# Performance work log

Hardware: AMD Instinct MI355X
Metric: run time of the kernel (lower is better)

## Reference

```python
import jax, jax.numpy as jnp
import numpy as np

D_MODEL = 2048
N_HEADS = 16
N_KV_HEADS = 4
HEAD_DIM = D_MODEL // N_HEADS  # 128
ROPE_THETA = 1000000.0


def _quant_rowwise(x):
    """Symmetric int8 rowwise quantization over the last dim (simulated in f32)."""
    s = jnp.max(jnp.abs(x), axis=-1, keepdims=True) / 127.0
    s = jnp.maximum(s, 1e-8)
    q = jnp.clip(jnp.round(x / s), -127.0, 127.0)
    return q, s


def _rope_tables(seq_len, head_dim, theta, dtype):
    inv_freq = 1.0 / (theta ** (jnp.arange(0, head_dim, 2, dtype=jnp.float32) / head_dim))
    pos = jnp.arange(seq_len, dtype=jnp.float32)
    freqs = pos[:, None] * inv_freq[None, :]            # (T, hd/2)
    emb = jnp.concatenate([freqs, freqs], axis=-1)      # (T, hd)
    return jnp.cos(emb).astype(dtype), jnp.sin(emb).astype(dtype)


def _rotate_half(x):
    h = x.shape[-1] // 2
    return jnp.concatenate([-x[..., h:], x[..., :h]], axis=-1)


def setup_inputs() -> dict:
    key = jax.random.key(0)
    k0, k1, k2, k3, k4 = jax.random.split(key, 5)
    x = jax.random.normal(k0, (1, 2048, D_MODEL), dtype=jnp.float32)
    sc = D_MODEL ** -0.5
    wq = jax.random.normal(k1, (N_HEADS * HEAD_DIM, D_MODEL), dtype=jnp.float32) * sc
    wk = jax.random.normal(k2, (N_KV_HEADS * HEAD_DIM, D_MODEL), dtype=jnp.float32) * sc
    wv = jax.random.normal(k3, (N_KV_HEADS * HEAD_DIM, D_MODEL), dtype=jnp.float32) * sc
    wo = jax.random.normal(k4, (D_MODEL, N_HEADS * HEAD_DIM), dtype=jnp.float32) * sc
    return {"x": x, "wq": wq, "wk": wk, "wv": wv, "wo": wo}


def _int8_linear(qx, x_scale, w):
    # Per-output-channel int8 weight quant, int8 matmul, rowwise dequant.
    qw, w_scale = _quant_rowwise(w)                      # (O,D), (O,1)
    y = jnp.einsum('btd,od->bto', qx, qw)
    return y * x_scale * w_scale[:, 0][None, None, :]


def reference(x, wq, wk, wv, wo):
    B, T, D = x.shape
    H, Hkv, hd = N_HEADS, N_KV_HEADS, HEAD_DIM
    scale = hd ** -0.5

    # Shared int8-quantized input for QKV projections
    qx, x_scale = _quant_rowwise(x)                      # (B,T,D), (B,T,1)
    q = _int8_linear(qx, x_scale, wq).reshape(B, T, H, hd).transpose(0, 2, 1, 3)
    k = _int8_linear(qx, x_scale, wk).reshape(B, T, Hkv, hd).transpose(0, 2, 1, 3)
    v = _int8_linear(qx, x_scale, wv).reshape(B, T, Hkv, hd).transpose(0, 2, 1, 3)

    # RoPE
    cos, sin = _rope_tables(T, hd, ROPE_THETA, x.dtype)  # (T, hd)
    q = q * cos + _rotate_half(q) * sin
    k = k * cos + _rotate_half(k) * sin

    # GQA: repeat kv heads
    rep = H // Hkv
    k = jnp.repeat(k, rep, axis=1)
    v = jnp.repeat(v, rep, axis=1)

    # int8 attention core: rowwise quantize q,k,v, int8 score matmul, dequant
    qq, qs = _quant_rowwise(q)
    kq, ks = _quant_rowwise(k)
    vq, vs = _quant_rowwise(v)
    scores = jnp.einsum('bhqd,bhkd->bhqk', qq, kq) * qs * jnp.swapaxes(ks, -1, -2) * scale
    causal = jnp.tril(jnp.ones((T, T), dtype=bool))
    scores = jnp.where(causal[None, None], scores, jnp.finfo(scores.dtype).min)
    attn = jax.nn.softmax(scores, axis=-1)
    out = jnp.einsum('bhqk,bhkd->bhqd', attn, vq * vs)   # dequant v inside matmul

    out = out.transpose(0, 2, 1, 3).reshape(B, T, H * hd)
    return out @ wo.T
```

## Files before the change

kernel.cpp:

```cpp
#include <hip/hip_runtime.h>
#include <cstdint>
#include <math.h>

#define TT 2048
#define DD 2048
#define NH 16
#define NKV 4
#define HD 128
#define SCALE_F 0.08838834764831845f
#define LOG2E 1.4426950408889634f

#if __has_builtin(__builtin_amdgcn_exp2f)
#define EXP2(x) __builtin_amdgcn_exp2f(x)
#else
#define EXP2(x) exp2f(x)
#endif

typedef int   i32x4 __attribute__((ext_vector_type(4)));
typedef float f32x4 __attribute__((ext_vector_type(4)));
typedef short s16x8 __attribute__((ext_vector_type(8)));

__device__ __forceinline__ i32x4 mfma_i8(i32x4 a, i32x4 b, i32x4 c) {
  return __builtin_amdgcn_mfma_i32_16x16x64_i8(a, b, c, 0, 0, 0);
}
__device__ __forceinline__ f32x4 mfma_bf16(s16x8 a, s16x8 b, f32x4 c) {
  return __builtin_amdgcn_mfma_f32_16x16x32_bf16(a, b, c, 0, 0, 0);
}
__device__ __forceinline__ uint32_t fbits(float f) {
  union { float f; uint32_t u; } x; x.f = f; return x.u;
}
__device__ __forceinline__ ushort bf16_rne(float v) {
  uint32_t u = fbits(v);
  return (ushort)((u + 0x7fffu + ((u >> 16) & 1u)) >> 16);
}
__device__ __forceinline__ float bf16_to_f(ushort h) {
  union { uint32_t u; float f; } x; x.u = ((uint32_t)h) << 16; return x.f;
}

__global__ __launch_bounds__(256)
void rope_table_kernel(float2* __restrict__ tab) {
  int idx = blockIdx.x * 256 + threadIdx.x;
  int t = idx >> 6, d = idx & 63;
  float inv = 1.0f / powf(1000000.0f, (float)d * (1.0f/64.0f));
  float ang = (float)t * inv;
  float sn, cs;
  sincosf(ang, &sn, &cs);
  tab[idx] = make_float2(cs, sn);
}

__global__ __launch_bounds__(256)
void quant_rows_kernel(const float* __restrict__ x, const float* __restrict__ wq,
                       const float* __restrict__ wk, const float* __restrict__ wv,
                       int8_t* __restrict__ qx, float* __restrict__ xs,
                       int8_t* __restrict__ qwq, float* __restrict__ wqs,
                       int8_t* __restrict__ qwk, float* __restrict__ wks,
                       int8_t* __restrict__ qwv, float* __restrict__ wvs) {
  int r = blockIdx.x;
  const float* src; int8_t* dst; float* sc; int row;
  if (r < 2048)      { src = x;  dst = qx;  sc = xs;  row = r; }
  else if (r < 4096) { src = wq; dst = qwq; sc = wqs; row = r - 2048; }
  else if (r < 4608) { src = wk; dst = qwk; sc = wks; row = r - 4096; }
  else               { src = wv; dst = qwv; sc = wvs; row = r - 4608; }
  src += (size_t)row * DD; dst += (size_t)row * DD;
  int tid = threadIdx.x;
  float4 v0 = ((const float4*)src)[2*tid];
  float4 v1 = ((const float4*)src)[2*tid+1];
  float m = fmaxf(fmaxf(fmaxf(fabsf(v0.x), fabsf(v0.y)), fmaxf(fabsf(v0.z), fabsf(v0.w))),
                  fmaxf(fmaxf(fabsf(v1.x), fabsf(v1.y)), fmaxf(fabsf(v1.z), fabsf(v1.w))));
  #pragma unroll
  for (int off = 1; off < 64; off <<= 1) m = fmaxf(m, __shfl_xor(m, off));
  __shared__ float wmax[4];
  if ((tid & 63) == 0) wmax[tid >> 6] = m;
  __syncthreads();
  m = fmaxf(fmaxf(wmax[0], wmax[1]), fmaxf(wmax[2], wmax[3]));
  float s = fmaxf(m / 127.0f, 1e-8f);
  if (tid == 0) sc[row] = s;
  float vv[8] = {v0.x, v0.y, v0.z, v0.w, v1.x, v1.y, v1.z, v1.w};
  uint32_t p0 = 0, p1 = 0;
  #pragma unroll
  for (int i = 0; i < 4; ++i) {
    int q = (int)fminf(fmaxf(rintf(vv[i] / s), -127.0f), 127.0f);
    p0 |= ((uint32_t)q & 0xffu) << (8*i);
  }
  #pragma unroll
  for (int i = 0; i < 4; ++i) {
    int q = (int)fminf(fmaxf(rintf(vv[4+i] / s), -127.0f), 127.0f);
    p1 |= ((uint32_t)q & 0xffu) << (8*i);
  }
  ((uint2*)dst)[tid] = make_uint2(p0, p1);
}

__global__ __launch_bounds__(128)
void proj_kernel(const int8_t* __restrict__ qx, const float* __restrict__ xs,
                 const int8_t* __restrict__ qwq, const float* __restrict__ wqs,
                 const int8_t* __restrict__ qwk, const float* __restrict__ wks,
                 const int8_t* __restrict__ qwv, const float* __restrict__ wvs,
                 const float2* __restrict__ ropet,
                 int8_t* __restrict__ qq, float* __restrict__ qsc_out,
                 int8_t* __restrict__ kq, float* __restrict__ ksc_out,
                 int8_t* __restrict__ vq, float* __restrict__ vsc_out) {
  int id  = blockIdx.x;
  int xcd = id & 7;
  int j   = id >> 3;
  int hg  = xcd >> 1;
  int th  = xcd & 1;
  int gh  = hg*6 + (j % 6);
  int tb  = th*16 + (j / 6);
  int t0  = tb * 64;

  const int8_t* wgt; const float* wsc; int8_t* outq; float* outs; bool doRope;
  if (gh < NH) {
    wgt = qwq + (size_t)gh*HD*DD; wsc = wqs + gh*HD;
    outq = qq + (size_t)gh*TT*HD; outs = qsc_out + (size_t)gh*TT; doRope = true;
  } else if (gh < NH + NKV) {
    int hh = gh - NH;
    wgt = qwk + (size_t)hh*HD*DD; wsc = wks + hh*HD;
    outq = kq + (size_t)hh*TT*HD; outs = ksc_out + (size_t)hh*TT; doRope = true;
  } else {
    int hh = gh - NH - NKV;
    wgt = qwv + (size_t)hh*HD*DD; wsc = wvs + hh*HD;
    outq = vq + (size_t)hh*TT*HD; outs = vsc_out + (size_t)hh*TT; doRope = false;
  }

  __shared__ int8_t As[64 * 144];
  __shared__ int8_t Bs[128 * 144];
  int tid = threadIdx.x;
  int w  = tid >> 6;
  int l  = tid & 63;
  int lg = l & 15;
  int lh = l >> 4;

  i32x4 acc[2][8];
  #pragma unroll
  for (int ti = 0; ti < 2; ++ti)
    #pragma unroll
    for (int tj = 0; tj < 8; ++tj) acc[ti][tj] = (i32x4){0,0,0,0};

  i32x4 prefA[4], prefB[8];

#define PROJ_ISSUE(KT)                                                          \
  {                                                                             \
    int kk0 = (KT) * 128;                                                       \
    _Pragma("unroll")                                                           \
    for (int i = 0; i < 4; ++i) {                                               \
      int idx = tid + i*128, r = idx >> 3, c = idx & 7;                         \
      prefA[i] = *(const i32x4*)&qx[(size_t)(t0 + r)*DD + kk0 + c*16];          \
    }                                                                           \
    _Pragma("unroll")                                                           \
    for (int i = 0; i < 8; ++i) {                                               \
      int idx = tid + i*128, r = idx >> 3, c = idx & 7;                         \
      prefB[i] = *(const i32x4*)&wgt[(size_t)r*DD + kk0 + c*16];                \
    }                                                                           \
  }

  PROJ_ISSUE(0);

  for (int kt = 0; kt < DD/128; ++kt) {
    __syncthreads();
    #pragma unroll
    for (int i = 0; i < 4; ++i) {
      int idx = tid + i*128, r = idx >> 3, c = idx & 7;
      *(i32x4*)&As[r*144 + c*16] = prefA[i];
    }
    #pragma unroll
    for (int i = 0; i < 8; ++i) {
      int idx = tid + i*128, r = idx >> 3, c = idx & 7;
      *(i32x4*)&Bs[r*144 + c*16] = prefB[i];
    }
    __syncthreads();
    if (kt + 1 < DD/128) PROJ_ISSUE(kt + 1);

    #pragma unroll
    for (int s = 0; s < 2; ++s) {
      i32x4 a0 = *(const i32x4*)&As[(w*32 + lg)*144      + s*64 + lh*16];
      i32x4 a1 = *(const i32x4*)&As[(w*32 + 16 + lg)*144 + s*64 + lh*16];
      #pragma unroll
      for (int tj = 0; tj < 8; ++tj) {
        i32x4 b = *(const i32x4*)&Bs[(tj*16 + lg)*144 + s*64 + lh*16];
        acc[0][tj] = mfma_i8(a0, b, acc[0][tj]);
        acc[1][tj] = mfma_i8(a1, b, acc[1][tj]);
      }
    }
  }
#undef PROJ_ISSUE

  float y[2][8][4];
  #pragma unroll
  for (int ti = 0; ti < 2; ++ti)
    #pragma unroll
    for (int rr = 0; rr < 4; ++rr) {
      int tl = w*32 + ti*16 + lh*4 + rr;
      float xsi = xs[t0 + tl];
      #pragma unroll
      for (int tj = 0; tj < 8; ++tj)
        y[ti][tj][rr] = (float)acc[ti][tj][rr] * xsi * wsc[tj*16 + lg];
    }

  if (doRope) {
    #pragma unroll
    for (int ti = 0; ti < 2; ++ti)
      #pragma unroll
      for (int rr = 0; rr < 4; ++rr) {
        int trow = t0 + w*32 + ti*16 + lh*4 + rr;
        const float2* tr = &ropet[trow * 64];
        #pragma unroll
        for (int tj = 0; tj < 4; ++tj) {
          float2 cssn = tr[tj*16 + lg];
          float lo = y[ti][tj][rr], hi = y[ti][tj+4][rr];
          y[ti][tj][rr]   = lo*cssn.x - hi*cssn.y;
          y[ti][tj+4][rr] = hi*cssn.x + lo*cssn.y;
        }
      }
  }

  __syncthreads();
  #pragma unroll
  for (int ti = 0; ti < 2; ++ti)
    #pragma unroll
    for (int rr = 0; rr < 4; ++rr) {
      int tl = w*32 + ti*16 + lh*4 + rr;
      float mx = fabsf(y[ti][0][rr]);
      #pragma unroll
      for (int tj = 1; tj < 8; ++tj) mx = fmaxf(mx, fabsf(y[ti][tj][rr]));
      mx = fmaxf(mx, __shfl_xor(mx, 1));
      mx = fmaxf(mx, __shfl_xor(mx, 2));
      mx = fmaxf(mx, __shfl_xor(mx, 4));
      mx = fmaxf(mx, __shfl_xor(mx, 8));
      float s = fmaxf(mx / 127.0f, 1e-8f);
      if (lg == 0) outs[t0 + tl] = s;
      #pragma unroll
      for (int tj = 0; tj < 8; ++tj) {
        int qv = (int)fminf(fmaxf(rintf(y[ti][tj][rr] / s), -127.0f), 127.0f);
        As[tl*144 + tj*16 + lg] = (int8_t)qv;
      }
    }
  __syncthreads();
  #pragma unroll
  for (int i = 0; i < 4; ++i) {
    int idx = tid + i*128, r = idx >> 3, c = idx & 7;
    *(i32x4*)&outq[(size_t)(t0 + r)*HD + c*16] = *(const i32x4*)&As[r*144 + c*16];
  }
}

__global__ __launch_bounds__(512)
void attn_mfma_kernel(const int8_t* __restrict__ qq, const float* __restrict__ qsc_in,
                      const int8_t* __restrict__ kq, const float* __restrict__ ksc_in,
                      const int8_t* __restrict__ vq, const float* __restrict__ vsc_in,
                      float* __restrict__ ao,
                      float* __restrict__ opA, float* __restrict__ opB,
                      float* __restrict__ ml) {
  int id = blockIdx.x;
  int h   = id / 30;
  int loc = id % 30;
  int qb2, c;
  if (loc < 12)      { qb2 = 15 - loc/3;        c = loc % 3; }
  else if (loc < 24) { qb2 = 11 - (loc - 12)/2; c = (loc - 12) % 2; }
  else               { qb2 = 5 - (loc - 24);    c = 0; }
  int nkt = 2*qb2 + 2;
  int nc  = (qb2 <= 5) ? 1 : ((qb2 <= 11) ? 2 : 3);
  int ktb = (c * nkt) / nc;
  int kte = ((c + 1) * nkt) / nc;
  int hk  = h >> 2;
  int qb0 = qb2 * 128;

  __shared__ int8_t Ks[64 * 144];
  __shared__ ushort Vt[128 * 72];

  int tid = threadIdx.x;
  int w  = tid >> 6;
  int l  = tid & 63;
  int lg = l & 15;
  int lh = l >> 4;

  const int8_t* qp = &qq[((size_t)h*TT + qb0 + 16*w + lg)*HD + lh*16];
  i32x4 qa0 = *(const i32x4*)qp;
  i32x4 qa1 = *(const i32x4*)(qp + 64);

  int myq = qb0 + 16*w + lg;
  float qsl = qsc_in[(size_t)h*TT + myq] * (SCALE_F * LOG2E);

  float mrun = -1e30f, lrun = 0.f;
  f32x4 acc_o[8];
  #pragma unroll
  for (int dt = 0; dt < 8; ++dt) acc_o[dt] = (f32x4){0.f, 0.f, 0.f, 0.f};

  int sr = tid >> 3, scc = tid & 7;
  int m2 = tid & 31, d0 = (tid >> 5) * 8;

  i32x4 kreg;
  int2  vreg0, vreg1;

#define ISSUE_LOADS(KT)                                                         \
  {                                                                             \
    int kk0 = (KT) * 64;                                                        \
    kreg = *(const i32x4*)&kq[((size_t)hk*TT + kk0 + sr)*HD + scc*16];          \
    const int8_t* vp = &vq[((size_t)hk*TT + kk0 + 2*m2)*HD + d0];               \
    vreg0 = *(const int2*)vp;                                                   \
    vreg1 = *(const int2*)(vp + HD);                                            \
  }

  ISSUE_LOADS(ktb);

  for (int kt = ktb; kt < kte; ++kt) {
    int k0 = kt * 64;
    __syncthreads();
    *(i32x4*)&Ks[sr*144 + scc*16] = kreg;
    #pragma unroll
    for (int jj = 0; jj < 4; ++jj) {
      int a0 = (vreg0.x << (24 - 8*jj)) >> 24;
      int b0 = (vreg1.x << (24 - 8*jj)) >> 24;
      *(uint32_t*)&Vt[(d0 + jj)*72 + 2*m2] =
          (fbits((float)a0) >> 16) | ((fbits((float)b0) >> 16) << 16);
      int a1 = (vreg0.y << (24 - 8*jj)) >> 24;
      int b1 = (vreg1.y << (24 - 8*jj)) >> 24;
      *(uint32_t*)&Vt[(d0 + 4 + jj)*72 + 2*m2] =
          (fbits((float)a1) >> 16) | ((fbits((float)b1) >> 16) << 16);
    }
    __syncthreads();
    if (kt + 1 < kte) ISSUE_LOADS(kt + 1);

    i32x4 sacc[4];
    #pragma unroll
    for (int t = 0; t < 4; ++t) sacc[t] = (i32x4){0, 0, 0, 0};
    __builtin_amdgcn_s_setprio(1);
    #pragma unroll
    for (int t = 0; t < 4; ++t) {
      const int8_t* kp = &Ks[(16*t + lg)*144 + lh*16];
      i32x4 b0 = *(const i32x4*)kp;
      i32x4 b1 = *(const i32x4*)(kp + 64);
      sacc[t] = mfma_i8(b0, qa0, sacc[t]);
      sacc[t] = mfma_i8(b1, qa1, sacc[t]);
    }
    __builtin_amdgcn_s_setprio(0);

    f32x4 ksv4[4], vsv4[4];
    #pragma unroll
    for (int t = 0; t < 4; ++t) {
      ksv4[t] = *(const f32x4*)&ksc_in[(size_t)hk*TT + k0 + 16*t + 4*lh];
      vsv4[t] = *(const f32x4*)&vsc_in[(size_t)hk*TT + k0 + 16*t + 4*lh];
    }

    bool maskTile = (kt >= nkt - 2);
    float sf[4][4];
    #pragma unroll
    for (int t = 0; t < 4; ++t)
      #pragma unroll
      for (int rr = 0; rr < 4; ++rr) {
        float v = (float)sacc[t][rr] * qsl * ksv4[t][rr];
        if (maskTile) {
          int kkg = k0 + 16*t + 4*lh + rr;
          v = (kkg <= myq) ? v : -1e30f;
        }
        sf[t][rr] = v;
      }

    float rm = sf[0][0];
    #pragma unroll
    for (int t = 0; t < 4; ++t)
      #pragma unroll
      for (int rr = 0; rr < 4; ++rr) rm = fmaxf(rm, sf[t][rr]);
    rm = fmaxf(rm, __shfl_xor(rm, 16));
    rm = fmaxf(rm, __shfl_xor(rm, 32));
    float mnew = fmaxf(mrun, rm);
    float corr = EXP2(mrun - mnew);
    mrun = mnew;
    float p[4][4];
    float ps = 0.f;
    #pragma unroll
    for (int t = 0; t < 4; ++t)
      #pragma unroll
      for (int rr = 0; rr < 4; ++rr) { p[t][rr] = EXP2(sf[t][rr] - mnew); ps += p[t][rr]; }
    ps += __shfl_xor(ps, 16);
    ps += __shfl_xor(ps, 32);
    lrun = lrun * corr + ps;

    float pp0[4], pp1[4], pp2[4], pp3[4];
    #pragma unroll
    for (int rr = 0; rr < 4; ++rr) {
      pp0[rr] = p[0][rr] * vsv4[0][rr];
      pp1[rr] = p[1][rr] * vsv4[1][rr];
      pp2[rr] = p[2][rr] * vsv4[2][rr];
      pp3[rr] = p[3][rr] * vsv4[3][rr];
    }

    #pragma unroll
    for (int dt = 0; dt < 8; ++dt)
      #pragma unroll
      for (int rr = 0; rr < 4; ++rr) acc_o[dt][rr] *= corr;

    int srcA = lg + ((l & 16) << 1);
    int srcB = srcA + 16;
    bool hiT = (lh >= 2);
    s16x8 pahi[2], palo[2];
    #pragma unroll
    for (int kb = 0; kb < 2; ++kb) {
      float xv[8];
      #pragma unroll
      for (int rr = 0; rr < 4; ++rr) {
        float loA = __shfl(kb == 0 ? pp0[rr] : pp2[rr], srcA);
        float hiA = __shfl(kb == 0 ? pp1[rr] : pp3[rr], srcA);
        float loB = __shfl(kb == 0 ? pp0[rr] : pp2[rr], srcB);
        float hiB = __shfl(kb == 0 ? pp1[rr] : pp3[rr], srcB);
        xv[rr]     = hiT ? hiA : loA;
        xv[4 + rr] = hiT ? hiB : loB;
      }
      float lv[8];
      #pragma unroll
      for (int jv = 0; jv < 8; ++jv) {
        uint32_t hb = fbits(xv[jv]) & 0xffff0000u;
        union { uint32_t u; float f; } hf; hf.u = hb;
        lv[jv] = xv[jv] - hf.f;
      }
      union { uint32_t u[4]; s16x8 v; } H, L;
      #pragma unroll
      for (int jj = 0; jj < 4; ++jj) {
        H.u[jj] = (fbits(xv[2*jj]) >> 16) | (fbits(xv[2*jj+1]) & 0xffff0000u);
        L.u[jj] = (fbits(lv[2*jj]) >> 16) | (fbits(lv[2*jj+1]) & 0xffff0000u);
      }
      pahi[kb] = H.v; palo[kb] = L.v;
    }

    __builtin_amdgcn_s_setprio(1);
    #pragma unroll
    for (int dt = 0; dt < 8; ++dt) {
      #pragma unroll
      for (int kb = 0; kb < 2; ++kb) {
        s16x8 vb = *(const s16x8*)&Vt[(16*dt + lg)*72 + kb*32 + lh*8];
        acc_o[dt] = mfma_bf16(vb, pahi[kb], acc_o[dt]);
        acc_o[dt] = mfma_bf16(vb, palo[kb], acc_o[dt]);
      }
    }
    __builtin_amdgcn_s_setprio(0);
  }
#undef ISSUE_LOADS

  if (nc == 1) {
    float invv = 1.0f / lrun;
    size_t base = (size_t)myq*DD + (size_t)h*HD;
    #pragma unroll
    for (int dt = 0; dt < 8; ++dt) {
      f32x4 v;
      #pragma unroll
      for (int rr = 0; rr < 4; ++rr) v[rr] = acc_o[dt][rr] * invv;
      *(f32x4*)&ao[base + 16*dt + 4*lh] = v;
    }
  } else {
    int base = (qb2 <= 11) ? (qb2 - 6)*2 : 12 + (qb2 - 12)*3;
    int slot = h*24 + base + c;
    float* op = (slot < 160) ? (opA + (size_t)slot * 16384)
                             : (opB + (size_t)(slot - 160) * 16384);
    op += (size_t)(16*w + lg) * 128;
    #pragma unroll
    for (int dt = 0; dt < 8; ++dt)
      *(f32x4*)&op[16*dt + 4*lh] = acc_o[dt];
    if (lh == 0) {
      ml[slot*256 + 16*w + lg]       = mrun;
      ml[slot*256 + 128 + 16*w + lg] = lrun;
    }
  }
}

__global__ __launch_bounds__(256)
void merge_kernel(const float* __restrict__ opA, const float* __restrict__ opB,
                  const float* __restrict__ ml,
                  float* __restrict__ ao) {
  int tile = blockIdx.x;
  int h = tile / 10;
  int qb2 = 6 + tile % 10;
  int nc = (qb2 <= 11) ? 2 : 3;
  int sbase = h*24 + ((qb2 <= 11) ? (qb2 - 6)*2 : 12 + (qb2 - 12)*3);

  int tid = threadIdx.x;
  int row = tid >> 1;
  int cseg = (tid & 1) * 64;

  float mv[3], lv[3];
  const float* pp[3];
  #pragma unroll
  for (int i = 0; i < 3; ++i) {
    int slot = sbase + ((i < nc) ? i : 0);
    const float* p = (slot < 160) ? (opA + (size_t)slot * 16384)
                                  : (opB + (size_t)(slot - 160) * 16384);
    pp[i] = p + (size_t)row * 128 + cseg;
    if (i < nc) {
      mv[i] = ml[slot*256 + row];
      lv[i] = ml[slot*256 + 128 + row];
    } else {
      mv[i] = -1e30f;
      lv[i] = 0.f;
    }
  }
  float M = fmaxf(fmaxf(mv[0], mv[1]), mv[2]);
  float wgt[3];
  float L = 0.f;
  #pragma unroll
  for (int i = 0; i < 3; ++i) { wgt[i] = EXP2(mv[i] - M); L += wgt[i]*lv[i]; }
  float inv = 1.0f / L;

  size_t ob = (size_t)(qb2*128 + row)*DD + (size_t)h*HD + cseg;
  #pragma unroll
  for (int c4 = 0; c4 < 16; ++c4) {
    f32x4 a0 = *(const f32x4*)&pp[0][c4*4];
    f32x4 a1 = *(const f32x4*)&pp[1][c4*4];
    f32x4 a2 = *(const f32x4*)&pp[2][c4*4];
    f32x4 v;
    #pragma unroll
    for (int e = 0; e < 4; ++e)
      v[e] = (wgt[0]*a0[e] + wgt[1]*a1[e] + wgt[2]*a2[e]) * inv;
    *(f32x4*)&ao[ob + c4*4] = v;
  }
}

__global__ __launch_bounds__(256)
void aquant_kernel(const float* __restrict__ ao,
                   int8_t* __restrict__ ahi, int8_t* __restrict__ alo,
                   float* __restrict__ sa) {
  int r = blockIdx.x;
  int tid = threadIdx.x;
  float4 a = ((const float4*)&ao[(size_t)r*DD])[2*tid];
  float4 b = ((const float4*)&ao[(size_t)r*DD])[2*tid+1];
  float v[8] = {a.x, a.y, a.z, a.w, b.x, b.y, b.z, b.w};
  float m = fabsf(v[0]);
  #pragma unroll
  for (int j = 1; j < 8; ++j) m = fmaxf(m, fabsf(v[j]));
  #pragma unroll
  for (int off = 1; off < 64; off <<= 1) m = fmaxf(m, __shfl_xor(m, off));
  __shared__ float wmax[4];
  if ((tid & 63) == 0) wmax[tid >> 6] = m;
  __syncthreads();
  m = fmaxf(fmaxf(wmax[0], wmax[1]), fmaxf(wmax[2], wmax[3]));
  float s = fmaxf(m * (1.0f/16256.0f), 1e-30f);
  if (tid == 0) sa[r] = s;
  float inv = 1.0f / s;
  uint32_t h0 = 0, h1 = 0, l0 = 0, l1 = 0;
  #pragma unroll
  for (int j = 0; j < 8; ++j) {
    float q = v[j] * inv;
    int hi = (int)fminf(fmaxf(rintf(q * (1.0f/128.0f)), -127.0f), 127.0f);
    int lo = (int)fminf(fmaxf(rintf(q - 128.0f*(float)hi), -127.0f), 127.0f);
    if (j < 4) { h0 |= ((uint32_t)hi & 0xffu) << (8*j);     l0 |= ((uint32_t)lo & 0xffu) << (8*j); }
    else       { h1 |= ((uint32_t)hi & 0xffu) << (8*(j-4)); l1 |= ((uint32_t)lo & 0xffu) << (8*(j-4)); }
  }
  ((uint2*)&ahi[(size_t)r*DD])[tid] = make_uint2(h0, h1);
  ((uint2*)&alo[(size_t)r*DD])[tid] = make_uint2(l0, l1);
}

__global__ __launch_bounds__(256)
void wquant_kernel(const float* __restrict__ wom,
                   int8_t* __restrict__ bhi, int8_t* __restrict__ blo,
                   float* __restrict__ sb) {
  int r = blockIdx.x;
  int tid = threadIdx.x;
  const float* src = wom + (size_t)r*DD + tid*8;
  float4 a = *(const float4*)src;
  float4 b = *(const float4*)(src + 4);
  float v[8] = {a.x, a.y, a.z, a.w, b.x, b.y, b.z, b.w};
  float m = fabsf(v[0]);
  #pragma unroll
  for (int j = 1; j < 8; ++j) m = fmaxf(m, fabsf(v[j]));
  #pragma unroll
  for (int off = 1; off < 64; off <<= 1) m = fmaxf(m, __shfl_xor(m, off));
  __shared__ float wmax[4];
  if ((tid & 63) == 0) wmax[tid >> 6] = m;
  __syncthreads();
  m = fmaxf(fmaxf(wmax[0], wmax[1]), fmaxf(wmax[2], wmax[3]));
  float s = fmaxf(m * (1.0f/16256.0f), 1e-30f);
  if (tid == 0) sb[r] = s;
  float inv = 1.0f / s;
  uint32_t h0 = 0, h1 = 0, l0 = 0, l1 = 0;
  #pragma unroll
  for (int j = 0; j < 8; ++j) {
    float q = v[j] * inv;
    int hi = (int)fminf(fmaxf(rintf(q * (1.0f/128.0f)), -127.0f), 127.0f);
    int lo = (int)fminf(fmaxf(rintf(q - 128.0f*(float)hi), -127.0f), 127.0f);
    if (j < 4) { h0 |= ((uint32_t)hi & 0xffu) << (8*j);     l0 |= ((uint32_t)lo & 0xffu) << (8*j); }
    else       { h1 |= ((uint32_t)hi & 0xffu) << (8*(j-4)); l1 |= ((uint32_t)lo & 0xffu) << (8*(j-4)); }
  }
  ((uint2*)&bhi[(size_t)r*DD])[tid] = make_uint2(h0, h1);
  ((uint2*)&blo[(size_t)r*DD])[tid] = make_uint2(l0, l1);
}

__global__ __launch_bounds__(256)
void wo_gemm_kernel(const int8_t* __restrict__ ahi, const int8_t* __restrict__ alo,
                    const int8_t* __restrict__ bhi, const int8_t* __restrict__ blo,
                    const float* __restrict__ sa, const float* __restrict__ sb,
                    float* __restrict__ outp) {
  int id  = blockIdx.x;
  int xcd = id & 7;
  int j   = id >> 3;
  int tb  = xcd*4 + (j >> 4);
  int ob  = j & 15;
  int t0  = tb * 64;
  int o0  = ob * 128;

  __shared__ int8_t AH[64 * 72];
  __shared__ int8_t AL[64 * 72];
  __shared__ int8_t BH[128 * 72];
  __shared__ int8_t BL[128 * 72];
  int tid = threadIdx.x;
  int wv4 = tid >> 6;
  int wr = wv4 >> 1, wc = wv4 & 1;
  int l  = tid & 63;
  int lg = l & 15;
  int lh = l >> 4;

  i32x4 acc_h[2][4], acc_m[2][4];
  #pragma unroll
  for (int ti = 0; ti < 2; ++ti)
    #pragma unroll
    for (int tj = 0; tj < 4; ++tj) {
      acc_h[ti][tj] = (i32x4){0,0,0,0};
      acc_m[ti][tj] = (i32x4){0,0,0,0};
    }

  i32x4 pAH, pAL, pBH[2], pBL[2];
  int ar = tid >> 2, ac = tid & 3;

#define WO_ISSUE(KT)                                                            \
  {                                                                             \
    int k0 = (KT) * 64;                                                         \
    size_t ga = (size_t)(t0 + ar)*DD + k0 + ac*16;                              \
    pAH = *(const i32x4*)&ahi[ga];                                              \
    pAL = *(const i32x4*)&alo[ga];                                              \
    _Pragma("unroll")                                                           \
    for (int i = 0; i < 2; ++i) {                                               \
      int idx = tid + i*256, r = idx >> 2, c = idx & 3;                         \
      size_t gb = (size_t)(o0 + r)*DD + k0 + c*16;                              \
      pBH[i] = *(const i32x4*)&bhi[gb];                                         \
      pBL[i] = *(const i32x4*)&blo[gb];                                         \
    }                                                                           \
  }

  WO_ISSUE(0);

  for (int kt = 0; kt < DD/64; ++kt) {
    __syncthreads();
    *(i32x4*)&AH[ar*72 + ac*16] = pAH;
    *(i32x4*)&AL[ar*72 + ac*16] = pAL;
    #pragma unroll
    for (int i = 0; i < 2; ++i) {
      int idx = tid + i*256, r = idx >> 2, c = idx & 3;
      *(i32x4*)&BH[r*72 + c*16] = pBH[i];
      *(i32x4*)&BL[r*72 + c*16] = pBL[i];
    }
    __syncthreads();
    if (kt + 1 < DD/64) WO_ISSUE(kt + 1);

    i32x4 a_h[2], a_l[2];
    #pragma unroll
    for (int ti = 0; ti < 2; ++ti) {
      int ab = (wr*32 + ti*16 + lg)*72 + lh*16;
      a_h[ti] = *(const i32x4*)&AH[ab];
      a_l[ti] = *(const i32x4*)&AL[ab];
    }
    __builtin_amdgcn_s_setprio(1);
    #pragma unroll
    for (int tj = 0; tj < 4; ++tj) {
      int bb = (wc*64 + tj*16 + lg)*72 + lh*16;
      i32x4 b_h = *(const i32x4*)&BH[bb];
      i32x4 b_l = *(const i32x4*)&BL[bb];
      #pragma unroll
      for (int ti = 0; ti < 2; ++ti) {
        acc_h[ti][tj] = mfma_i8(a_h[ti], b_h, acc_h[ti][tj]);
        acc_m[ti][tj] = mfma_i8(a_h[ti], b_l, acc_m[ti][tj]);
        acc_m[ti][tj] = mfma_i8(a_l[ti], b_h, acc_m[ti][tj]);
      }
    }
    __builtin_amdgcn_s_setprio(0);
  }
#undef WO_ISSUE

  #pragma unroll
  for (int ti = 0; ti < 2; ++ti) {
    float sav[4];
    #pragma unroll
    for (int rr = 0; rr < 4; ++rr)
      sav[rr] = sa[t0 + wr*32 + ti*16 + lh*4 + rr];
    #pragma unroll
    for (int tj = 0; tj < 4; ++tj) {
      int o = o0 + wc*64 + tj*16 + lg;
      float sbo = sb[o];
      #pragma unroll
      for (int rr = 0; rr < 4; ++rr) {
        int t = t0 + wr*32 + ti*16 + lh*4 + rr;
        float v = sav[rr] * sbo *
                  (16384.0f * (float)acc_h[ti][tj][rr] + 128.0f * (float)acc_m[ti][tj][rr]);
        outp[(size_t)t*DD + o] = v;
      }
    }
  }
}

extern "C" void kernel_launch(void* const* d_in, const int* in_sizes, int n_in,
                              void* d_out, int out_size, void* d_ws, size_t ws_size,
                              hipStream_t stream) {
  (void)in_sizes; (void)n_in; (void)out_size; (void)ws_size;
  const float* x  = (const float*)d_in[0];
  const float* wq = (const float*)d_in[1];
  const float* wk = (const float*)d_in[2];
  const float* wv = (const float*)d_in[3];
  const float* wo = (const float*)d_in[4];
  float* out = (float*)d_out;

  char* ws = (char*)d_ws;
  const size_t MB = 1048576;
  int8_t* qx  = (int8_t*)(ws);
  int8_t* qwq = (int8_t*)(ws + 4*MB);
  int8_t* qwk = (int8_t*)(ws + 8*MB);
  int8_t* qwv = (int8_t*)(ws + 9*MB);
  int8_t* qqp = (int8_t*)(ws + 10*MB);
  int8_t* kqp = (int8_t*)(ws + 14*MB);
  int8_t* vqp = (int8_t*)(ws + 15*MB);
  float* xs  = (float*)(ws + 16*MB);
  float* wqs = xs + 2048;
  float* wks = wqs + 2048;
  float* wvs = wks + 512;
  float* qsc = wvs + 512;
  float* ksc = qsc + (size_t)NH*TT;
  float* vsc = ksc + (size_t)NKV*TT;
  float* ao = (float*)(ws + 16*MB + 262144);
  float2* ropet = (float2*)(ws + 16*MB + 262144);
  float* opA = (float*)(ws);
  float* opB = out;
  float* mlb = (float*)((char*)out + 15*MB + 524288);
  int8_t* ahi = (int8_t*)(ws);
  int8_t* alo = (int8_t*)(ws + 4*MB);
  int8_t* bhi = (int8_t*)(ws + 8*MB);
  int8_t* blo = (int8_t*)(ws + 12*MB);
  float* sa = (float*)(ws + 16*MB);
  float* sb = sa + 2048;

  rope_table_kernel<<<512, 256, 0, stream>>>(ropet);
  quant_rows_kernel<<<5120, 256, 0, stream>>>(x, wq, wk, wv,
                                              qx, xs, qwq, wqs, qwk, wks, qwv, wvs);
  proj_kernel<<<768, 128, 0, stream>>>(
      qx, xs, qwq, wqs, qwk, wks, qwv, wvs, ropet,
      qqp, qsc, kqp, ksc, vqp, vsc);
  attn_mfma_kernel<<<480, 512, 0, stream>>>(
      qqp, qsc, kqp, ksc, vqp, vsc, ao, opA, opB, mlb);
  merge_kernel<<<160, 256, 0, stream>>>(opA, opB, mlb, ao);
  aquant_kernel<<<2048, 256, 0, stream>>>(ao, ahi, alo, sa);
  wquant_kernel<<<2048, 256, 0, stream>>>(wo, bhi, blo, sb);
  wo_gemm_kernel<<<512, 256, 0, stream>>>(ahi, alo, bhi, blo, sa, sb, out);
}
```

Measured before the change: 168.0 us.

## Fuse small prep kernels, widen projection blocks, stage attention P through LDS

The RoPE table build is folded into the quant_rows launch as extra blocks, and the activation and weight quantization kernels are merged into one launch, removing two kernel launches. The projection kernel moves from 128 to 256 threads per block, so each wave computes 16 rows instead of 32, which lowers per-thread register pressure and raises the wave count. In attention, the P-tile layout shuffle for the PV MFMA now goes through a per-wave LDS buffer instead of many cross-lane shuffles. This costs extra LDS capacity and LDS traffic, which may reduce attention occupancy.

```diff
diff --git a/kernel.cpp b/kernel.cpp
--- a/kernel.cpp
+++ b/kernel.cpp
@@ -29,23 +29,8 @@
 __device__ __forceinline__ uint32_t fbits(float f) {
   union { float f; uint32_t u; } x; x.f = f; return x.u;
 }
-__device__ __forceinline__ ushort bf16_rne(float v) {
-  uint32_t u = fbits(v);
-  return (ushort)((u + 0x7fffu + ((u >> 16) & 1u)) >> 16);
-}
 __device__ __forceinline__ float bf16_to_f(ushort h) {
   union { uint32_t u; float f; } x; x.u = ((uint32_t)h) << 16; return x.f;
-}
-
-__global__ __launch_bounds__(256)
-void rope_table_kernel(float2* __restrict__ tab) {
-  int idx = blockIdx.x * 256 + threadIdx.x;
-  int t = idx >> 6, d = idx & 63;
-  float inv = 1.0f / powf(1000000.0f, (float)d * (1.0f/64.0f));
-  float ang = (float)t * inv;
-  float sn, cs;
-  sincosf(ang, &sn, &cs);
-  tab[idx] = make_float2(cs, sn);
 }
 
 __global__ __launch_bounds__(256)
@@ -54,15 +39,25 @@
                        int8_t* __restrict__ qx, float* __restrict__ xs,
                        int8_t* __restrict__ qwq, float* __restrict__ wqs,
                        int8_t* __restrict__ qwk, float* __restrict__ wks,
-                       int8_t* __restrict__ qwv, float* __restrict__ wvs) {
+                       int8_t* __restrict__ qwv, float* __restrict__ wvs,
+                       float2* __restrict__ ropet) {
   int r = blockIdx.x;
+  int tid = threadIdx.x;
+  if (r >= 5120) {
+    int idx = (r - 5120) * 256 + tid;
+    int t = idx >> 6, d = idx & 63;
+    float inv = 1.0f / powf(1000000.0f, (float)d * (1.0f/64.0f));
+    float sn, cs;
+    sincosf((float)t * inv, &sn, &cs);
+    ropet[idx] = make_float2(cs, sn);
+    return;
+  }
   const float* src; int8_t* dst; float* sc; int row;
   if (r < 2048)      { src = x;  dst = qx;  sc = xs;  row = r; }
   else if (r < 4096) { src = wq; dst = qwq; sc = wqs; row = r - 2048; }
   else if (r < 4608) { src = wk; dst = qwk; sc = wks; row = r - 4096; }
   else               { src = wv; dst = qwv; sc = wvs; row = r - 4608; }
   src += (size_t)row * DD; dst += (size_t)row * DD;
-  int tid = threadIdx.x;
   float4 v0 = ((const float4*)src)[2*tid];
   float4 v1 = ((const float4*)src)[2*tid+1];
   float m = fmaxf(fmaxf(fmaxf(fabsf(v0.x), fabsf(v0.y)), fmaxf(fabsf(v0.z), fabsf(v0.w))),
@@ -90,7 +85,7 @@
   ((uint2*)dst)[tid] = make_uint2(p0, p1);
 }
 
-__global__ __launch_bounds__(128)
+__global__ __launch_bounds__(256)
 void proj_kernel(const int8_t* __restrict__ qx, const float* __restrict__ xs,
                  const int8_t* __restrict__ qwq, const float* __restrict__ wqs,
                  const int8_t* __restrict__ qwk, const float* __restrict__ wks,
@@ -130,25 +125,23 @@
   int lg = l & 15;
   int lh = l >> 4;
 
-  i32x4 acc[2][8];
-  #pragma unroll
-  for (int ti = 0; ti < 2; ++ti)
-    #pragma unroll
-    for (int tj = 0; tj < 8; ++tj) acc[ti][tj] = (i32x4){0,0,0,0};
-
-  i32x4 prefA[4], prefB[8];
+  i32x4 acc[8];
+  #pragma unroll
+  for (int tj = 0; tj < 8; ++tj) acc[tj] = (i32x4){0,0,0,0};
+
+  i32x4 prefA[2], prefB[4];
 
 #define PROJ_ISSUE(KT)                                                          \
   {                                                                             \
     int kk0 = (KT) * 128;                                                       \
     _Pragma("unroll")                                                           \
-    for (int i = 0; i < 4; ++i) {                                               \
-      int idx = tid + i*128, r = idx >> 3, c = idx & 7;                         \
+    for (int i = 0; i < 2; ++i) {                                               \
+      int idx = tid + i*256, r = idx >> 3, c = idx & 7;                         \
       prefA[i] = *(const i32x4*)&qx[(size_t)(t0 + r)*DD + kk0 + c*16];          \
     }                                                                           \
     _Pragma("unroll")                                                           \
-    for (int i = 0; i < 8; ++i) {                                               \
-      int idx = tid + i*128, r = idx >> 3, c = idx & 7;                         \
+    for (int i = 0; i < 4; ++i) {                                               \
+      int idx = tid + i*256, r = idx >> 3, c = idx & 7;                         \
       prefB[i] = *(const i32x4*)&wgt[(size_t)r*DD + kk0 + c*16];                \
     }                                                                           \
   }
@@ -158,13 +151,13 @@
   for (int kt = 0; kt < DD/128; ++kt) {
     __syncthreads();
     #pragma unroll
+    for (int i = 0; i < 2; ++i) {
+      int idx = tid + i*256, r = idx >> 3, c = idx & 7;
+      *(i32x4*)&As[r*144 + c*16] = prefA[i];
+    }
+    #pragma unroll
     for (int i = 0; i < 4; ++i) {
-      int idx = tid + i*128, r = idx >> 3, c = idx & 7;
-      *(i32x4*)&As[r*144 + c*16] = prefA[i];
-    }
-    #pragma unroll
-    for (int i = 0; i < 8; ++i) {
-      int idx = tid + i*128, r = idx >> 3, c = idx & 7;
+      int idx = tid + i*256, r = idx >> 3, c = idx & 7;
       *(i32x4*)&Bs[r*144 + c*16] = prefB[i];
     }
     __syncthreads();
@@ -172,72 +165,64 @@
 
     #pragma unroll
     for (int s = 0; s < 2; ++s) {
-      i32x4 a0 = *(const i32x4*)&As[(w*32 + lg)*144      + s*64 + lh*16];
-      i32x4 a1 = *(const i32x4*)&As[(w*32 + 16 + lg)*144 + s*64 + lh*16];
+      i32x4 a0 = *(const i32x4*)&As[(w*16 + lg)*144 + s*64 + lh*16];
       #pragma unroll
       for (int tj = 0; tj < 8; ++tj) {
         i32x4 b = *(const i32x4*)&Bs[(tj*16 + lg)*144 + s*64 + lh*16];
-        acc[0][tj] = mfma_i8(a0, b, acc[0][tj]);
-        acc[1][tj] = mfma_i8(a1, b, acc[1][tj]);
+        acc[tj] = mfma_i8(a0, b, acc[tj]);
       }
     }
   }
 #undef PROJ_ISSUE
 
-  float y[2][8][4];
-  #pragma unroll
-  for (int ti = 0; ti < 2; ++ti)
+  float y[8][4];
+  #pragma unroll
+  for (int rr = 0; rr < 4; ++rr) {
+    int tl = w*16 + lh*4 + rr;
+    float xsi = xs[t0 + tl];
+    #pragma unroll
+    for (int tj = 0; tj < 8; ++tj)
+      y[tj][rr] = (float)acc[tj][rr] * xsi * wsc[tj*16 + lg];
+  }
+
+  if (doRope) {
     #pragma unroll
     for (int rr = 0; rr < 4; ++rr) {
-      int tl = w*32 + ti*16 + lh*4 + rr;
-      float xsi = xs[t0 + tl];
-      #pragma unroll
-      for (int tj = 0; tj < 8; ++tj)
-        y[ti][tj][rr] = (float)acc[ti][tj][rr] * xsi * wsc[tj*16 + lg];
-    }
-
-  if (doRope) {
-    #pragma unroll
-    for (int ti = 0; ti < 2; ++ti)
-      #pragma unroll
-      for (int rr = 0; rr < 4; ++rr) {
-        int trow = t0 + w*32 + ti*16 + lh*4 + rr;
-        const float2* tr = &ropet[trow * 64];
-        #pragma unroll
-        for (int tj = 0; tj < 4; ++tj) {
-          float2 cssn = tr[tj*16 + lg];
-          float lo = y[ti][tj][rr], hi = y[ti][tj+4][rr];
-          y[ti][tj][rr]   = lo*cssn.x - hi*cssn.y;
-          y[ti][tj+4][rr] = hi*cssn.x + lo*cssn.y;
-        }
-      }
+      int trow = t0 + w*16 + lh*4 + rr;
+      const float2* tr = &ropet[trow * 64];
+      #pragma unroll
+      for (int tj = 0; tj < 4; ++tj) {
+        float2 cssn = tr[tj*16 + lg];
+        float lo = y[tj][rr], hi = y[tj+4][rr];
+        y[tj][rr]   = lo*cssn.x - hi*cssn.y;
+        y[tj+4][rr] = hi*cssn.x + lo*cssn.y;
+      }
+    }
   }
 
   __syncthreads();
   #pragma unroll
-  for (int ti = 0; ti < 2; ++ti)
-    #pragma unroll
-    for (int rr = 0; rr < 4; ++rr) {
-      int tl = w*32 + ti*16 + lh*4 + rr;
-      float mx = fabsf(y[ti][0][rr]);
-      #pragma unroll
-      for (int tj = 1; tj < 8; ++tj) mx = fmaxf(mx, fabsf(y[ti][tj][rr]));
-      mx = fmaxf(mx, __shfl_xor(mx, 1));
-      mx = fmaxf(mx, __shfl_xor(mx, 2));
-      mx = fmaxf(mx, __shfl_xor(mx, 4));
-      mx = fmaxf(mx, __shfl_xor(mx, 8));
-      float s = fmaxf(mx / 127.0f, 1e-8f);
-      if (lg == 0) outs[t0 + tl] = s;
-      #pragma unroll
-      for (int tj = 0; tj < 8; ++tj) {
-        int qv = (int)fminf(fmaxf(rintf(y[ti][tj][rr] / s), -127.0f), 127.0f);
-        As[tl*144 + tj*16 + lg] = (int8_t)qv;
-      }
-    }
+  for (int rr = 0; rr < 4; ++rr) {
+    int tl = w*16 + lh*4 + rr;
+    float mx = fabsf(y[0][rr]);
+    #pragma unroll
+    for (int tj = 1; tj < 8; ++tj) mx = fmaxf(mx, fabsf(y[tj][rr]));
+    mx = fmaxf(mx, __shfl_xor(mx, 1));
+    mx = fmaxf(mx, __shfl_xor(mx, 2));
+    mx = fmaxf(mx, __shfl_xor(mx, 4));
+    mx = fmaxf(mx, __shfl_xor(mx, 8));
+    float s = fmaxf(mx / 127.0f, 1e-8f);
+    if (lg == 0) outs[t0 + tl] = s;
+    #pragma unroll
+    for (int tj = 0; tj < 8; ++tj) {
+      int qv = (int)fminf(fmaxf(rintf(y[tj][rr] / s), -127.0f), 127.0f);
+      As[tl*144 + tj*16 + lg] = (int8_t)qv;
+    }
+  }
   __syncthreads();
   #pragma unroll
-  for (int i = 0; i < 4; ++i) {
-    int idx = tid + i*128, r = idx >> 3, c = idx & 7;
+  for (int i = 0; i < 2; ++i) {
+    int idx = tid + i*256, r = idx >> 3, c = idx & 7;
     *(i32x4*)&outq[(size_t)(t0 + r)*HD + c*16] = *(const i32x4*)&As[r*144 + c*16];
   }
 }
@@ -265,6 +250,7 @@
 
   __shared__ int8_t Ks[64 * 144];
   __shared__ ushort Vt[128 * 72];
+  __shared__ float  Pf[8][16 * 68];
 
   int tid = threadIdx.x;
   int w  = tid >> 6;
@@ -374,13 +360,12 @@
     ps += __shfl_xor(ps, 32);
     lrun = lrun * corr + ps;
 
-    float pp0[4], pp1[4], pp2[4], pp3[4];
-    #pragma unroll
-    for (int rr = 0; rr < 4; ++rr) {
-      pp0[rr] = p[0][rr] * vsv4[0][rr];
-      pp1[rr] = p[1][rr] * vsv4[1][rr];
-      pp2[rr] = p[2][rr] * vsv4[2][rr];
-      pp3[rr] = p[3][rr] * vsv4[3][rr];
+    #pragma unroll
+    for (int t = 0; t < 4; ++t) {
+      f32x4 pw;
+      #pragma unroll
+      for (int rr = 0; rr < 4; ++rr) pw[rr] = p[t][rr] * vsv4[t][rr];
+      *(f32x4*)&Pf[w][lg*68 + 16*t + 4*lh] = pw;
     }
 
     #pragma unroll
@@ -388,22 +373,13 @@
       #pragma unroll
       for (int rr = 0; rr < 4; ++rr) acc_o[dt][rr] *= corr;
 
-    int srcA = lg + ((l & 16) << 1);
-    int srcB = srcA + 16;
-    bool hiT = (lh >= 2);
     s16x8 pahi[2], palo[2];
     #pragma unroll
     for (int kb = 0; kb < 2; ++kb) {
-      float xv[8];
-      #pragma unroll
-      for (int rr = 0; rr < 4; ++rr) {
-        float loA = __shfl(kb == 0 ? pp0[rr] : pp2[rr], srcA);
-        float hiA = __shfl(kb == 0 ? pp1[rr] : pp3[rr], srcA);
-        float loB = __shfl(kb == 0 ? pp0[rr] : pp2[rr], srcB);
-        float hiB = __shfl(kb == 0 ? pp1[rr] : pp3[rr], srcB);
-        xv[rr]     = hiT ? hiA : loA;
-        xv[4 + rr] = hiT ? hiB : loB;
-      }
+      const float* pr = &Pf[w][lg*68 + kb*32 + lh*8];
+      f32x4 x0 = *(const f32x4*)pr;
+      f32x4 x1 = *(const f32x4*)(pr + 4);
+      float xv[8] = {x0.x, x0.y, x0.z, x0.w, x1.x, x1.y, x1.z, x1.w};
       float lv[8];
       #pragma unroll
       for (int jv = 0; jv < 8; ++jv) {
@@ -512,13 +488,18 @@
 }
 
 __global__ __launch_bounds__(256)
-void aquant_kernel(const float* __restrict__ ao,
-                   int8_t* __restrict__ ahi, int8_t* __restrict__ alo,
-                   float* __restrict__ sa) {
+void awquant_kernel(const float* __restrict__ ao, const float* __restrict__ wom,
+                    int8_t* __restrict__ ahi, int8_t* __restrict__ alo,
+                    int8_t* __restrict__ bhi, int8_t* __restrict__ blo,
+                    float* __restrict__ sa, float* __restrict__ sb) {
   int r = blockIdx.x;
   int tid = threadIdx.x;
-  float4 a = ((const float4*)&ao[(size_t)r*DD])[2*tid];
-  float4 b = ((const float4*)&ao[(size_t)r*DD])[2*tid+1];
+  const float* src; int8_t* dhi; int8_t* dlo; float* sc; int row;
+  if (r < 2048) { src = ao;  dhi = ahi; dlo = alo; sc = sa; row = r; }
+  else          { src = wom; dhi = bhi; dlo = blo; sc = sb; row = r - 2048; }
+  src += (size_t)row * DD;
+  float4 a = ((const float4*)src)[2*tid];
+  float4 b = ((const float4*)src)[2*tid+1];
   float v[8] = {a.x, a.y, a.z, a.w, b.x, b.y, b.z, b.w};
   float m = fabsf(v[0]);
   #pragma unroll
@@ -530,7 +511,7 @@
   __syncthreads();
   m = fmaxf(fmaxf(wmax[0], wmax[1]), fmaxf(wmax[2], wmax[3]));
   float s = fmaxf(m * (1.0f/16256.0f), 1e-30f);
-  if (tid == 0) sa[r] = s;
+  if (tid == 0) sc[row] = s;
   float inv = 1.0f / s;
   uint32_t h0 = 0, h1 = 0, l0 = 0, l1 = 0;
   #pragma unroll
@@ -541,43 +522,8 @@
     if (j < 4) { h0 |= ((uint32_t)hi & 0xffu) << (8*j);     l0 |= ((uint32_t)lo & 0xffu) << (8*j); }
     else       { h1 |= ((uint32_t)hi & 0xffu) << (8*(j-4)); l1 |= ((uint32_t)lo & 0xffu) << (8*(j-4)); }
   }
-  ((uint2*)&ahi[(size_t)r*DD])[tid] = make_uint2(h0, h1);
-  ((uint2*)&alo[(size_t)r*DD])[tid] = make_uint2(l0, l1);
-}
-
-__global__ __launch_bounds__(256)
-void wquant_kernel(const float* __restrict__ wom,
-                   int8_t* __restrict__ bhi, int8_t* __restrict__ blo,
-                   float* __restrict__ sb) {
-  int r = blockIdx.x;
-  int tid = threadIdx.x;
-  const float* src = wom + (size_t)r*DD + tid*8;
-  float4 a = *(const float4*)src;
-  float4 b = *(const float4*)(src + 4);
-  float v[8] = {a.x, a.y, a.z, a.w, b.x, b.y, b.z, b.w};
-  float m = fabsf(v[0]);
-  #pragma unroll
-  for (int j = 1; j < 8; ++j) m = fmaxf(m, fabsf(v[j]));
-  #pragma unroll
-  for (int off = 1; off < 64; off <<= 1) m = fmaxf(m, __shfl_xor(m, off));
-  __shared__ float wmax[4];
-  if ((tid & 63) == 0) wmax[tid >> 6] = m;
-  __syncthreads();
-  m = fmaxf(fmaxf(wmax[0], wmax[1]), fmaxf(wmax[2], wmax[3]));
-  float s = fmaxf(m * (1.0f/16256.0f), 1e-30f);
-  if (tid == 0) sb[r] = s;
-  float inv = 1.0f / s;
-  uint32_t h0 = 0, h1 = 0, l0 = 0, l1 = 0;
-  #pragma unroll
-  for (int j = 0; j < 8; ++j) {
-    float q = v[j] * inv;
-    int hi = (int)fminf(fmaxf(rintf(q * (1.0f/128.0f)), -127.0f), 127.0f);
-    int lo = (int)fminf(fmaxf(rintf(q - 128.0f*(float)hi), -127.0f), 127.0f);
-    if (j < 4) { h0 |= ((uint32_t)hi & 0xffu) << (8*j);     l0 |= ((uint32_t)lo & 0xffu) << (8*j); }
-    else       { h1 |= ((uint32_t)hi & 0xffu) << (8*(j-4)); l1 |= ((uint32_t)lo & 0xffu) << (8*(j-4)); }
-  }
-  ((uint2*)&bhi[(size_t)r*DD])[tid] = make_uint2(h0, h1);
-  ((uint2*)&blo[(size_t)r*DD])[tid] = make_uint2(l0, l1);
+  ((uint2*)&dhi[(size_t)row*DD])[tid] = make_uint2(h0, h1);
+  ((uint2*)&dlo[(size_t)row*DD])[tid] = make_uint2(l0, l1);
 }
 
 __global__ __launch_bounds__(256)
@@ -730,16 +676,15 @@
   float* sa = (float*)(ws + 16*MB);
   float* sb = sa + 2048;
 
-  rope_table_kernel<<<512, 256, 0, stream>>>(ropet);
-  quant_rows_kernel<<<5120, 256, 0, stream>>>(x, wq, wk, wv,
-                                              qx, xs, qwq, wqs, qwk, wks, qwv, wvs);
-  proj_kernel<<<768, 128, 0, stream>>>(
+  quant_rows_kernel<<<5632, 256, 0, stream>>>(x, wq, wk, wv,
+                                              qx, xs, qwq, wqs, qwk, wks, qwv, wvs,
+                                              ropet);
+  proj_kernel<<<768, 256, 0, stream>>>(
       qx, xs, qwq, wqs, qwk, wks, qwv, wvs, ropet,
       qqp, qsc, kqp, ksc, vqp, vsc);
   attn_mfma_kernel<<<480, 512, 0, stream>>>(
       qqp, qsc, kqp, ksc, vqp, vsc, ao, opA, opB, mlb);
   merge_kernel<<<160, 256, 0, stream>>>(opA, opB, mlb, ao);
-  aquant_kernel<<<2048, 256, 0, stream>>>(ao, ahi, alo, sa);
-  wquant_kernel<<<2048, 256, 0, stream>>>(wo, bhi, blo, sb);
+  awquant_kernel<<<4096, 256, 0, stream>>>(ao, wo, ahi, alo, bhi, blo, sa, sb);
   wo_gemm_kernel<<<512, 256, 0, stream>>>(ahi, alo, bhi, blo, sa, sb, out);
 }
```

After: 152.4 us. 1.1x faster.
